# Kernel tuning notes

Hardware: AMD Instinct MI355X
Metric: run time of the kernel (lower is better)

## Reference

```python
import jax, jax.numpy as jnp
import numpy as np

E = 200      # embsize
R = 480      # num relations
T = 8        # cur_ts (history length)
N = 40000    # num entities
B = 1024     # batch of triples
NEG_INF = -1.0e9


def _lin(x, W, b):
    # torch nn.Linear convention: y = x @ W.T + b
    return x @ W.T + b


def _gru_cell(x, h, wih, whh, bih, bhh):
    # torch GRUCell: gates packed as [r, z, n]
    gi = x @ wih.T + bih
    gh = h @ whh.T + bhh
    i_r, i_z, i_n = jnp.split(gi, 3, axis=1)
    h_r, h_z, h_n = jnp.split(gh, 3, axis=1)
    r = jax.nn.sigmoid(i_r + h_r)
    z = jax.nn.sigmoid(i_z + h_z)
    n = jnp.tanh(i_n + r * h_n)
    return (1.0 - z) * n + z * h


def setup_inputs() -> dict:
    key = jax.random.key(0)
    ks = jax.random.split(key, 24)
    s = 0.05
    pre_emb = jax.random.normal(ks[0], (N, E), dtype=jnp.float32)
    r_emb = jax.random.normal(ks[1], (R, E), dtype=jnp.float32)
    partial_embeding = jax.random.randint(ks[2], (B, T * R), 0, 2).astype(jnp.float32)
    sub = jax.random.randint(ks[3], (B,), 0, N)
    rel = jax.random.randint(ks[4], (B,), 0, R)
    obj = jax.random.randint(ks[5], (B,), 0, N)
    all_triples = jnp.stack([sub, rel, obj], axis=1).astype(jnp.int64)
    params = {
        'W1': jax.random.normal(ks[6], (2 * E, E)) * s, 'b1': jnp.zeros((2 * E,)),
        'W2': jax.random.normal(ks[7], (E, 2 * E)) * s, 'b2': jnp.zeros((E,)),
        'Wa': jax.random.normal(ks[8], (E, E)) * s, 'ba': jnp.zeros((E,)),
        'Wh1': jax.random.normal(ks[9], (E, E)) * s, 'bh1': jnp.zeros((E,)),
        'Wh2': jax.random.normal(ks[10], (E, E)) * s, 'bh2': jnp.zeros((E,)),
        'Wal': jax.random.normal(ks[11], (E, E)) * s, 'bal': jnp.zeros((E,)),
        'gru_wih': jax.random.normal(ks[12], (3 * E, E)) * s,
        'gru_whh': jax.random.normal(ks[13], (3 * E, E)) * s,
        'gru_bih': jnp.zeros((3 * E,)),
        'gru_bhh': jnp.zeros((3 * E,)),
    }
    params = {k: v.astype(jnp.float32) for k, v in params.items()}
    out = {'pre_emb': pre_emb, 'r_emb': r_emb, 'partial_embeding': partial_embeding,
           'all_triples': all_triples, 'cur_ts': T, 'num_rel': R}
    out.update(params)
    return out


def reference(pre_emb, r_emb, partial_embeding, all_triples, cur_ts, num_rel,
              W1, b1, W2, b2, Wa, ba, Wh1, bh1, Wh2, bh2, Wal, bal,
              gru_wih, gru_whh, gru_bih, gru_bhh):
    mapped_rel = _lin(_lin(r_emb, W1, b1), W2, b2)          # [R, E]
    q_rel = mapped_rel[all_triples[:, 1]]                    # [B, E]
    b = partial_embeding.shape[0]

    # loop-invariant attention base: linear_attn(q_rel) @ mapped_rel^T -> [B, R]
    base = _lin(q_rel, Wa, ba) @ mapped_rel.T

    # [B, cur_ts*R] -> [cur_ts, B, R] for scan over timesteps
    pe = partial_embeding.reshape(b, cur_ts, num_rel).transpose(1, 0, 2)

    def step(h, cur):
        attn = cur * base
        attn = jnp.where(attn == 0, jnp.float32(NEG_INF), attn)
        a = jax.nn.softmax(attn, axis=1)
        x = a @ mapped_rel                                   # [B, E]
        h = _gru_cell(x, h, gru_wih, gru_whh, gru_bih, gru_bhh)
        return h, None

    h0 = jnp.zeros((b, mapped_rel.shape[1]), dtype=pre_emb.dtype)
    gru_hidden, _ = jax.lax.scan(step, h0, pe)

    predicted_hist = 0.1 * _lin(_lin(q_rel, Wh1, bh1), Wh2, bh2) + q_rel
    match_loss = jnp.mean((predicted_hist - gru_hidden) ** 2)

    # forward_forth (distmult scoring)
    gru_hidden2 = _gru_cell(q_rel, predicted_hist, gru_wih, gru_whh, gru_bih, gru_bhh)
    sub_emb = pre_emb[all_triples[:, 0]]
    score_logits = (_lin(sub_emb, Wal, bal) * gru_hidden2) @ _lin(pre_emb, Wal, bal).T  # [B, N]
    score = jax.nn.sigmoid(score_logits)

    labels = jnp.zeros_like(score_logits).at[jnp.arange(b), all_triples[:, 2]].set(1.0)
    # stable BCE(sigmoid(s), y)
    path_loss = -jnp.mean(labels * jax.nn.log_sigmoid(score_logits)
                          + (1.0 - labels) * jax.nn.log_sigmoid(-score_logits))
    return (match_loss, path_loss, score)
```

## Files before the change

### kernel.cpp

```cpp
#include <hip/hip_runtime.h>
#include <hip/hip_bf16.h>
#include <math.h>

#define EE 200
#define RR 480
#define TT 8
#define NN 40000
#define BB 1024
#define KP 224
#define GP 672
#define GPR 704
#define LDS_STRIDE 232

typedef __attribute__((ext_vector_type(8))) short short8v;
typedef __attribute__((ext_vector_type(4))) float f32x4;

__device__ inline unsigned short f2bf(float x) {
    unsigned int u = __float_as_uint(x);
    unsigned int r = ((u >> 16) & 1u) + 0x7fffu;
    return (unsigned short)((u + r) >> 16);
}
__device__ inline float bf2f(unsigned short h) {
    return __uint_as_float(((unsigned int)h) << 16);
}
__device__ inline float sigm(float x) { return 1.0f / (1.0f + __expf(-x)); }
__device__ inline void split_store(unsigned short* hi, unsigned short* lo, size_t i, float v) {
    unsigned short h = f2bf(v);
    hi[i] = h;
    lo[i] = f2bf(v - bf2f(h));
}

__global__ __launch_bounds__(256) void prep_kernel(
    const float* __restrict__ W1, const float* __restrict__ W2,
    const float* __restrict__ Wa, const float* __restrict__ Wh1,
    const float* __restrict__ Wh2, const float* __restrict__ Wal,
    const float* __restrict__ bal, const float* __restrict__ wih,
    const float* __restrict__ whh, const float* __restrict__ bih,
    const float* __restrict__ bhh,
    unsigned short* W1h, unsigned short* W1l,
    unsigned short* W2h, unsigned short* W2l,
    unsigned short* Wah, unsigned short* Wal_,
    unsigned short* Wh1h, unsigned short* Wh1l,
    unsigned short* Wh2h, unsigned short* Wh2l,
    unsigned short* Walh, unsigned short* Wall,
    unsigned short* WTh, unsigned short* WTl,
    unsigned short* wgh, unsigned short* wgl,
    unsigned short* whg, unsigned short* whl,
    float* bihp, float* bhhp,
    unsigned short* mapSh, unsigned short* mapSl,
    unsigned short* wgiSh, unsigned short* wgiSl,
    unsigned short* hbufs, double* acc)
{
    const int gt = blockIdx.x * 256 + threadIdx.x;
    const int gs = gridDim.x * 256;

    for (int i = gt; i < 448 * 224; i += gs) {
        int r = i / 224, c = i - r * 224;
        split_store(W1h, W1l, i, (r < 400 && c < 200) ? W1[r * 200 + c] : 0.f);
    }
    for (int i = gt; i < 256 * 416; i += gs) {
        int r = i / 416, c = i - r * 416;
        split_store(W2h, W2l, i, (r < 200 && c < 400) ? W2[r * 400 + c] : 0.f);
    }
    for (int i = gt; i < 256 * 224; i += gs) {
        int r = i / 224, c = i - r * 224;
        bool in = (r < 200 && c < 200);
        split_store(Wah,  Wal_, i, in ? Wa[r * 200 + c]  : 0.f);
        split_store(Wh1h, Wh1l, i, in ? Wh1[r * 200 + c] : 0.f);
        split_store(Wh2h, Wh2l, i, in ? Wh2[r * 200 + c] : 0.f);
        split_store(Walh, Wall, i, in ? Wal[r * 200 + c] : 0.f);
        float vt = in ? Wal[c * 200 + r] : ((r == 200 && c < 200) ? bal[c] : 0.f);
        split_store(WTh, WTl, i, vt);
    }
    for (int i = gt; i < 672 * 224; i += gs) {
        int rr = i / 224, c = i - rr * 224;
        int g = rr / 224, j = rr - g * 224;
        bool in = (j < 200 && c < 200);
        split_store(wgh, wgl, i, in ? wih[(size_t)(g * 200 + j) * 200 + c] : 0.f);
        split_store(whg, whl, i, in ? whh[(size_t)(g * 200 + j) * 200 + c] : 0.f);
    }
    for (int i = gt; i < GPR; i += gs) {
        int g = i / 224, j = i - g * 224;
        bihp[i] = (g < 3 && j < 200) ? bih[g * 200 + j] : 0.f;
    }
    for (int i = gt; i < GP; i += gs) {
        int g = i / 224, j = i - g * 224;
        bhhp[i] = (j < 200) ? bhh[g * 200 + j] : 0.f;
    }
    for (int i = gt; i < 512 * 224; i += gs) { mapSh[i] = 0; mapSl[i] = 0; }
    for (int i = gt; i < 704 * 480; i += gs) { wgiSh[i] = 0; wgiSl[i] = 0; }
    for (int i = gt; i < 4 * BB * KP; i += gs) hbufs[i] = 0;
    if (gt == 0) { acc[0] = 0.0; acc[1] = 0.0; }
}

template <int MODE, int OUT, int GATHER, int GATEPAD>
__global__ __launch_bounds__(256) void mfma_flyA(
    const float* __restrict__ A, const int* __restrict__ gidx, int gsel,
    const unsigned short* __restrict__ Bhi, const unsigned short* __restrict__ Blo,
    const float* __restrict__ bias,
    float* __restrict__ Cf, unsigned short* __restrict__ Chi, unsigned short* __restrict__ Clo,
    int M, int N, int Ka, int Ks,
    const float* __restrict__ extra, float alpha, int obf)
{
    const int tid = threadIdx.x;
    const int wave = tid >> 6, lane = tid & 63;
    const int r16 = lane & 15, kq = lane >> 4;
    const int kbase = kq * 8;
    const int bm = blockIdx.y * 64 + wave * 16;
    const int bn = blockIdx.x * 64;

    int arow = bm + r16;
    const bool avalid = arow < M;
    if (GATHER) { if (avalid) arow = gidx[arow * 3 + gsel]; }
    const float* Ap = A + (size_t)arow * Ka;

    f32x4 acc[4] = {{0,0,0,0},{0,0,0,0},{0,0,0,0},{0,0,0,0}};
    const int nk = Ks >> 5;

    for (int kk = 0; kk < nk; kk++) {
        const int k0 = kk * 32 + kbase;
        short8v a0, a1;
        #pragma unroll
        for (int e = 0; e < 8; e++) {
            float v = (avalid && (k0 + e) < Ka) ? Ap[k0 + e] : 0.f;
            unsigned short h = f2bf(v);
            a0[e] = (short)h;
            a1[e] = (short)f2bf(v - bf2f(h));
        }
        #pragma unroll
        for (int nf = 0; nf < 4; nf++) {
            const size_t boff = (size_t)(bn + nf * 16 + r16) * Ks + k0;
            short8v b0 = *(const short8v*)(Bhi + boff);
            short8v b1 = *(const short8v*)(Blo + boff);
            acc[nf] = __builtin_amdgcn_mfma_f32_16x16x32_bf16(a0, b1, acc[nf], 0, 0, 0);
            acc[nf] = __builtin_amdgcn_mfma_f32_16x16x32_bf16(a1, b0, acc[nf], 0, 0, 0);
            acc[nf] = __builtin_amdgcn_mfma_f32_16x16x32_bf16(a0, b0, acc[nf], 0, 0, 0);
        }
    }

    #pragma unroll
    for (int r = 0; r < 4; r++) {
        const int orow = bm + kq * 4 + r;
        if (orow >= M) continue;
        #pragma unroll
        for (int nf = 0; nf < 4; nf++) {
            const int col = bn + nf * 16 + r16;
            float v = acc[nf][r];
            if (OUT == 0) {
                if (col < N) {
                    if (bias) v += bias[col];
                    if (MODE == 1) v = alpha * v + extra[(size_t)orow * N + col];
                    else if (MODE == 2) v = v * extra[(size_t)orow * N + col];
                    Cf[(size_t)orow * N + col] = v;
                }
            } else if (OUT == 1) {
                if (col < obf) {
                    float w = 0.f;
                    if (col < N) { w = v; if (bias) w += bias[col]; }
                    Chi[(size_t)orow * obf + col] = f2bf(w);
                }
            } else if (OUT == 2) {
                if (col < N) {
                    int wr = GATEPAD ? (orow / 200) * 224 + orow % 200 : orow;
                    if (bias) v += bias[col];
                    split_store(Chi, Clo, (size_t)wr * obf + col, v);
                }
            } else if (OUT == 3) {
                if (col < N) {
                    if (bias) v += bias[col];
                    Cf[(size_t)orow * N + col] = v;
                    split_store(Chi, Clo, (size_t)orow * obf + col, v);
                }
            }
        }
    }
}

__global__ __launch_bounds__(256) void mfma_linear3_kernel(
    const unsigned short* __restrict__ Ahi, const unsigned short* __restrict__ Alo,
    const unsigned short* __restrict__ Bhi, const unsigned short* __restrict__ Blo,
    const float* __restrict__ bias, float* __restrict__ C,
    int M, int N, int Ks)
{
    const int tid  = threadIdx.x;
    const int wave = tid >> 6;
    const int lane = tid & 63;
    const int r16   = lane & 15;
    const int khalf = lane >> 4;
    const int kbase = khalf * 8;
    const int bm = blockIdx.y * 64 + wave * 16;
    const int bn = blockIdx.x * 64;

    const unsigned short* ah = Ahi + (size_t)(bm + r16) * Ks + kbase;
    const unsigned short* al = Alo + (size_t)(bm + r16) * Ks + kbase;
    const unsigned short* bh = Bhi + (size_t)(bn + r16) * Ks + kbase;
    const unsigned short* bl = Blo + (size_t)(bn + r16) * Ks + kbase;

    f32x4 acc[4] = {{0,0,0,0},{0,0,0,0},{0,0,0,0},{0,0,0,0}};

    for (int k0 = 0; k0 < Ks; k0 += 32) {
        short8v a0 = *(const short8v*)(ah + k0);
        short8v a1 = *(const short8v*)(al + k0);
        #pragma unroll
        for (int nf = 0; nf < 4; nf++) {
            short8v b0 = *(const short8v*)(bh + (size_t)nf * 16 * Ks + k0);
            short8v b1 = *(const short8v*)(bl + (size_t)nf * 16 * Ks + k0);
            acc[nf] = __builtin_amdgcn_mfma_f32_16x16x32_bf16(a0, b1, acc[nf], 0, 0, 0);
            acc[nf] = __builtin_amdgcn_mfma_f32_16x16x32_bf16(a1, b0, acc[nf], 0, 0, 0);
            acc[nf] = __builtin_amdgcn_mfma_f32_16x16x32_bf16(a0, b0, acc[nf], 0, 0, 0);
        }
    }
    #pragma unroll
    for (int r = 0; r < 4; r++) {
        const int row = bm + khalf * 4 + r;
        #pragma unroll
        for (int nf = 0; nf < 4; nf++) {
            const int col = bn + nf * 16 + r16;
            if (col < N)
                C[(size_t)row * N + col] = acc[nf][r] + (bias ? bias[col] : 0.0f);
        }
    }
}

template <int LAST>
__global__ __launch_bounds__(256) void gru_step_kernel(
    const unsigned short* __restrict__ Whi, const unsigned short* __restrict__ Wlo,
    const float* __restrict__ bhh_pad,
    const float* __restrict__ gi_t,
    const unsigned short* __restrict__ hin_hi, const unsigned short* __restrict__ hin_lo,
    unsigned short* __restrict__ hout_hi, unsigned short* __restrict__ hout_lo,
    float* __restrict__ h_fin)
{
    const int tid = threadIdx.x;
    const int wave = tid >> 6, lane = tid & 63;
    const int r16 = lane & 15, kq = lane >> 4;
    const int jf = blockIdx.x;
    const int brow = (blockIdx.y * 4 + wave) * 16;
    const int j = jf * 16 + r16;

    short8v ahi[7], alo[7];
    const unsigned short* hh = hin_hi + (size_t)(brow + r16) * KP + kq * 8;
    const unsigned short* hl = hin_lo + (size_t)(brow + r16) * KP + kq * 8;
    #pragma unroll
    for (int kk = 0; kk < 7; kk++) {
        ahi[kk] = *(const short8v*)(hh + kk * 32);
        alo[kk] = *(const short8v*)(hl + kk * 32);
    }

    f32x4 ar = {0,0,0,0}, az = {0,0,0,0}, an = {0,0,0,0};
    #pragma unroll
    for (int kk = 0; kk < 7; kk++) {
        const size_t rowr = (size_t)(jf * 16 + r16) * KP + kk * 32 + kq * 8;
        const size_t rowz = rowr + (size_t)224 * KP;
        const size_t rown = rowr + (size_t)448 * KP;
        short8v brh = *(const short8v*)(Whi + rowr);
        short8v brl = *(const short8v*)(Wlo + rowr);
        short8v bzh = *(const short8v*)(Whi + rowz);
        short8v bzl = *(const short8v*)(Wlo + rowz);
        short8v bnh = *(const short8v*)(Whi + rown);
        short8v bnl = *(const short8v*)(Wlo + rown);
        ar = __builtin_amdgcn_mfma_f32_16x16x32_bf16(ahi[kk], brl, ar, 0, 0, 0);
        az = __builtin_amdgcn_mfma_f32_16x16x32_bf16(ahi[kk], bzl, az, 0, 0, 0);
        an = __builtin_amdgcn_mfma_f32_16x16x32_bf16(ahi[kk], bnl, an, 0, 0, 0);
        ar = __builtin_amdgcn_mfma_f32_16x16x32_bf16(alo[kk], brh, ar, 0, 0, 0);
        az = __builtin_amdgcn_mfma_f32_16x16x32_bf16(alo[kk], bzh, az, 0, 0, 0);
        an = __builtin_amdgcn_mfma_f32_16x16x32_bf16(alo[kk], bnh, an, 0, 0, 0);
        ar = __builtin_amdgcn_mfma_f32_16x16x32_bf16(ahi[kk], brh, ar, 0, 0, 0);
        az = __builtin_amdgcn_mfma_f32_16x16x32_bf16(ahi[kk], bzh, az, 0, 0, 0);
        an = __builtin_amdgcn_mfma_f32_16x16x32_bf16(ahi[kk], bnh, an, 0, 0, 0);
    }

    const float br = bhh_pad[j], bz = bhh_pad[224 + j], bn_ = bhh_pad[448 + j];
    #pragma unroll
    for (int q = 0; q < 4; q++) {
        const int row = brow + kq * 4 + q;
        float gir = gi_t[(size_t)row * GP + j];
        float giz = gi_t[(size_t)row * GP + 224 + j];
        float gin = gi_t[(size_t)row * GP + 448 + j];
        float r_ = sigm(gir + ar[q] + br);
        float z_ = sigm(giz + az[q] + bz);
        float n_ = tanhf(gin + r_ * (an[q] + bn_));
        float hold = bf2f(hin_hi[(size_t)row * KP + j]) + bf2f(hin_lo[(size_t)row * KP + j]);
        float hnew = (1.0f - z_) * n_ + z_ * hold;
        if (j < EE) {
            unsigned short nh = f2bf(hnew);
            hout_hi[(size_t)row * KP + j] = nh;
            hout_lo[(size_t)row * KP + j] = f2bf(hnew - bf2f(nh));
            if (LAST) h_fin[(size_t)row * EE + j] = hnew;
        }
    }
}

__global__ __launch_bounds__(256) void gru2_fused_kernel(
    const unsigned short* __restrict__ Wihi, const unsigned short* __restrict__ Wilo,
    const unsigned short* __restrict__ Whhi, const unsigned short* __restrict__ Whlo,
    const float* __restrict__ bih_pad, const float* __restrict__ bhh_pad,
    const float* __restrict__ x, const float* __restrict__ hp,
    float* __restrict__ ghid2)
{
    const int tid = threadIdx.x;
    const int wave = tid >> 6, lane = tid & 63;
    const int r16 = lane & 15, kq = lane >> 4;
    const int jf = blockIdx.x;
    const int brow = (blockIdx.y * 4 + wave) * 16;
    const int j = jf * 16 + r16;

    f32x4 ir = {0,0,0,0}, iz = {0,0,0,0}, in_ = {0,0,0,0};
    f32x4 hr = {0,0,0,0}, hz = {0,0,0,0}, hn = {0,0,0,0};

    {
        const float* xp = x + (size_t)(brow + r16) * EE;
        #pragma unroll
        for (int kk = 0; kk < 7; kk++) {
            short8v a0, a1;
            #pragma unroll
            for (int e = 0; e < 8; e++) {
                int k = kk * 32 + kq * 8 + e;
                float v = (k < EE) ? xp[k] : 0.0f;
                unsigned short hhh = f2bf(v);
                a0[e] = (short)hhh;
                a1[e] = (short)f2bf(v - bf2f(hhh));
            }
            const size_t rowr = (size_t)(jf * 16 + r16) * KP + kk * 32 + kq * 8;
            const size_t rowz = rowr + (size_t)224 * KP;
            const size_t rown = rowr + (size_t)448 * KP;
            short8v brh = *(const short8v*)(Wihi + rowr);
            short8v brl = *(const short8v*)(Wilo + rowr);
            short8v bzh = *(const short8v*)(Wihi + rowz);
            short8v bzl = *(const short8v*)(Wilo + rowz);
            short8v bnh = *(const short8v*)(Wihi + rown);
            short8v bnl = *(const short8v*)(Wilo + rown);
            ir = __builtin_amdgcn_mfma_f32_16x16x32_bf16(a0, brl, ir, 0, 0, 0);
            iz = __builtin_amdgcn_mfma_f32_16x16x32_bf16(a0, bzl, iz, 0, 0, 0);
            in_ = __builtin_amdgcn_mfma_f32_16x16x32_bf16(a0, bnl, in_, 0, 0, 0);
            ir = __builtin_amdgcn_mfma_f32_16x16x32_bf16(a1, brh, ir, 0, 0, 0);
            iz = __builtin_amdgcn_mfma_f32_16x16x32_bf16(a1, bzh, iz, 0, 0, 0);
            in_ = __builtin_amdgcn_mfma_f32_16x16x32_bf16(a1, bnh, in_, 0, 0, 0);
            ir = __builtin_amdgcn_mfma_f32_16x16x32_bf16(a0, brh, ir, 0, 0, 0);
            iz = __builtin_amdgcn_mfma_f32_16x16x32_bf16(a0, bzh, iz, 0, 0, 0);
            in_ = __builtin_amdgcn_mfma_f32_16x16x32_bf16(a0, bnh, in_, 0, 0, 0);
        }
    }
    {
        const float* hpp = hp + (size_t)(brow + r16) * EE;
        #pragma unroll
        for (int kk = 0; kk < 7; kk++) {
            short8v a0, a1;
            #pragma unroll
            for (int e = 0; e < 8; e++) {
                int k = kk * 32 + kq * 8 + e;
                float v = (k < EE) ? hpp[k] : 0.0f;
                unsigned short hhh = f2bf(v);
                a0[e] = (short)hhh;
                a1[e] = (short)f2bf(v - bf2f(hhh));
            }
            const size_t rowr = (size_t)(jf * 16 + r16) * KP + kk * 32 + kq * 8;
            const size_t rowz = rowr + (size_t)224 * KP;
            const size_t rown = rowr + (size_t)448 * KP;
            short8v brh = *(const short8v*)(Whhi + rowr);
            short8v brl = *(const short8v*)(Whlo + rowr);
            short8v bzh = *(const short8v*)(Whhi + rowz);
            short8v bzl = *(const short8v*)(Whlo + rowz);
            short8v bnh = *(const short8v*)(Whhi + rown);
            short8v bnl = *(const short8v*)(Whlo + rown);
            hr = __builtin_amdgcn_mfma_f32_16x16x32_bf16(a0, brl, hr, 0, 0, 0);
            hz = __builtin_amdgcn_mfma_f32_16x16x32_bf16(a0, bzl, hz, 0, 0, 0);
            hn = __builtin_amdgcn_mfma_f32_16x16x32_bf16(a0, bnl, hn, 0, 0, 0);
            hr = __builtin_amdgcn_mfma_f32_16x16x32_bf16(a1, brh, hr, 0, 0, 0);
            hz = __builtin_amdgcn_mfma_f32_16x16x32_bf16(a1, bzh, hz, 0, 0, 0);
            hn = __builtin_amdgcn_mfma_f32_16x16x32_bf16(a1, bnh, hn, 0, 0, 0);
            hr = __builtin_amdgcn_mfma_f32_16x16x32_bf16(a0, brh, hr, 0, 0, 0);
            hz = __builtin_amdgcn_mfma_f32_16x16x32_bf16(a0, bzh, hz, 0, 0, 0);
            hn = __builtin_amdgcn_mfma_f32_16x16x32_bf16(a0, bnh, hn, 0, 0, 0);
        }
    }

    if (j >= EE) return;
    const float bir = bih_pad[j], biz = bih_pad[224 + j], bin = bih_pad[448 + j];
    const float bhr = bhh_pad[j], bhz = bhh_pad[224 + j], bhn = bhh_pad[448 + j];
    #pragma unroll
    for (int q = 0; q < 4; q++) {
        const int row = brow + kq * 4 + q;
        float r_ = sigm(ir[q] + bir + hr[q] + bhr);
        float z_ = sigm(iz[q] + biz + hz[q] + bhz);
        float n_ = tanhf(in_[q] + bin + r_ * (hn[q] + bhn));
        float hold = hp[(size_t)row * EE + j];
        ghid2[(size_t)row * EE + j] = (1.0f - z_) * n_ + z_ * hold;
    }
}

__global__ __launch_bounds__(256) void score_mfma2_kernel(
    const unsigned short* __restrict__ Ubf,
    const float* __restrict__ pre_emb,
    const int* __restrict__ triples,
    float* __restrict__ outScore,
    double* __restrict__ accPath)
{
    __shared__ unsigned short Bs[64 * LDS_STRIDE];
    __shared__ int objs[BB];
    __shared__ float red[256];

    const int tid = threadIdx.x;
    const int bn = blockIdx.x * 64;

    for (int i = tid; i < BB; i += 256) objs[i] = triples[i * 3 + 2];

    for (int idx = tid; idx < 64 * 50; idx += 256) {
        int row = idx / 50;
        int c4 = (idx - row * 50) * 4;
        float4 v = *(const float4*)(pre_emb + (size_t)(bn + row) * EE + c4);
        unsigned short* d = &Bs[row * LDS_STRIDE + c4];
        d[0] = f2bf(v.x); d[1] = f2bf(v.y); d[2] = f2bf(v.z); d[3] = f2bf(v.w);
    }
    for (int idx = tid; idx < 64 * 24; idx += 256) {
        int row = idx / 24;
        int cc = idx - row * 24;
        Bs[row * LDS_STRIDE + 200 + cc] = (cc == 0) ? (unsigned short)0x3F80 : (unsigned short)0;
    }
    __syncthreads();

    const int wave  = tid >> 6;
    const int lane  = tid & 63;
    const int r16   = lane & 15;
    const int khalf = lane >> 4;
    const int kbase = khalf * 8;

    const unsigned short* bs0 = &Bs[( 0 + r16) * LDS_STRIDE + kbase];
    const unsigned short* bs1 = &Bs[(16 + r16) * LDS_STRIDE + kbase];
    const unsigned short* bs2 = &Bs[(32 + r16) * LDS_STRIDE + kbase];
    const unsigned short* bs3 = &Bs[(48 + r16) * LDS_STRIDE + kbase];

    float psum = 0.0f;

    for (int m0 = 0; m0 < BB; m0 += 64) {
        const unsigned short* Ap = Ubf + (size_t)(m0 + wave * 16 + r16) * KP + kbase;
        f32x4 acc0 = {0,0,0,0}, acc1 = {0,0,0,0}, acc2 = {0,0,0,0}, acc3 = {0,0,0,0};
        #pragma unroll
        for (int k0 = 0; k0 < KP; k0 += 32) {
            short8v a  = *(const short8v*)(Ap + k0);
            short8v b0 = *(const short8v*)(bs0 + k0);
            short8v b1 = *(const short8v*)(bs1 + k0);
            short8v b2 = *(const short8v*)(bs2 + k0);
            short8v b3 = *(const short8v*)(bs3 + k0);
            acc0 = __builtin_amdgcn_mfma_f32_16x16x32_bf16(a, b0, acc0, 0, 0, 0);
            acc1 = __builtin_amdgcn_mfma_f32_16x16x32_bf16(a, b1, acc1, 0, 0, 0);
            acc2 = __builtin_amdgcn_mfma_f32_16x16x32_bf16(a, b2, acc2, 0, 0, 0);
            acc3 = __builtin_amdgcn_mfma_f32_16x16x32_bf16(a, b3, acc3, 0, 0, 0);
        }
        #pragma unroll
        for (int r = 0; r < 4; r++) {
            const int grow = m0 + wave * 16 + khalf * 4 + r;
            const int objc = objs[grow];
            float xv[4] = { acc0[r], acc1[r], acc2[r], acc3[r] };
            #pragma unroll
            for (int nf = 0; nf < 4; nf++) {
                const int col = bn + nf * 16 + r16;
                float x  = xv[nf];
                float e  = __expf(-fabsf(x));
                float t1 = 1.0f + e;
                float rc = __builtin_amdgcn_rcpf(t1);
                float sig = (x >= 0.0f) ? rc : e * rc;
                float sp = __logf(t1);
                float s  = (col == objc) ? x : -x;
                psum += fminf(s, 0.0f) - sp;
                outScore[(size_t)grow * NN + col] = sig;
            }
        }
    }
    red[tid] = psum;
    __syncthreads();
    for (int s = 128; s > 0; s >>= 1) {
        if (tid < s) red[tid] += red[tid + s];
        __syncthreads();
    }
    if (tid == 0) atomicAdd(accPath, (double)red[0]);
}

__global__ __launch_bounds__(256) void masked_softmax_all_kernel(
    const float* __restrict__ base, const float* __restrict__ part,
    unsigned short* __restrict__ aout_hi, unsigned short* __restrict__ aout_lo)
{
    __shared__ float sv[RR];
    __shared__ float red[256];
    const int blk = blockIdx.x;
    const int b = blk & (BB - 1);
    const int t = blk >> 10;
    const int tid = threadIdx.x;
    const float* brow = base + (size_t)b * RR;
    const float* prow = part + (size_t)b * (TT * RR) + t * RR;

    float lmax = -3.0e38f;
    for (int r = tid; r < RR; r += 256) {
        float v = prow[r] * brow[r];
        if (v == 0.0f) v = -1000000000.0f;
        sv[r] = v;
        lmax = fmaxf(lmax, v);
    }
    red[tid] = lmax;
    __syncthreads();
    for (int s = 128; s > 0; s >>= 1) {
        if (tid < s) red[tid] = fmaxf(red[tid], red[tid + s]);
        __syncthreads();
    }
    float gmax = red[0];
    __syncthreads();

    float lsum = 0.0f;
    for (int r = tid; r < RR; r += 256) {
        float e = __expf(sv[r] - gmax);
        sv[r] = e;
        lsum += e;
    }
    red[tid] = lsum;
    __syncthreads();
    for (int s = 128; s > 0; s >>= 1) {
        if (tid < s) red[tid] += red[tid + s];
        __syncthreads();
    }
    float inv = 1.0f / red[0];
    for (int r = tid; r < RR; r += 256) {
        float w = sv[r] * inv;
        unsigned short h = f2bf(w);
        aout_hi[(size_t)blk * RR + r] = h;
        aout_lo[(size_t)blk * RR + r] = f2bf(w - bf2f(h));
    }
}

__global__ __launch_bounds__(256) void gather_rows_kernel(
    const float* __restrict__ src, const int* __restrict__ idx,
    int idxStride, int idxOff, float* __restrict__ dst, int rows, int cols)
{
    int i = blockIdx.x * 256 + threadIdx.x;
    if (i >= rows * cols) return;
    int r = i / cols, c = i - r * cols;
    dst[i] = src[(size_t)idx[r * idxStride + idxOff] * cols + c];
}

__global__ __launch_bounds__(256) void sqdiff_reduce_kernel(
    const float* __restrict__ a, const float* __restrict__ b, int n,
    double* __restrict__ acc)
{
    __shared__ float red[256];
    int tid = threadIdx.x;
    float s = 0.0f;
    for (int i = blockIdx.x * 256 + tid; i < n; i += gridDim.x * 256) {
        float d = a[i] - b[i];
        s += d * d;
    }
    red[tid] = s;
    __syncthreads();
    for (int st = 128; st > 0; st >>= 1) {
        if (tid < st) red[tid] += red[tid + st];
        __syncthreads();
    }
    if (tid == 0) atomicAdd(acc, (double)red[0]);
}

__global__ void final_kernel(const double* __restrict__ acc, float* __restrict__ out)
{
    if (threadIdx.x == 0) {
        out[0] = (float)(acc[0] / ((double)BB * EE));
        out[1] = (float)(-acc[1] / ((double)BB * NN));
    }
}

extern "C" void kernel_launch(void* const* d_in, const int* in_sizes, int n_in,
                              void* d_out, int out_size, void* d_ws, size_t ws_size,
                              hipStream_t stream) {
    const float* pre_emb = (const float*)d_in[0];
    const float* r_emb   = (const float*)d_in[1];
    const float* part    = (const float*)d_in[2];
    const int*   triples = (const int*)d_in[3];
    const float* W1  = (const float*)d_in[6];
    const float* b1  = (const float*)d_in[7];
    const float* W2  = (const float*)d_in[8];
    const float* b2  = (const float*)d_in[9];
    const float* Wa  = (const float*)d_in[10];
    const float* ba  = (const float*)d_in[11];
    const float* Wh1 = (const float*)d_in[12];
    const float* bh1 = (const float*)d_in[13];
    const float* Wh2 = (const float*)d_in[14];
    const float* bh2 = (const float*)d_in[15];
    const float* Wal = (const float*)d_in[16];
    const float* bal = (const float*)d_in[17];
    const float* wih = (const float*)d_in[18];
    const float* whh = (const float*)d_in[19];
    const float* bih = (const float*)d_in[20];
    const float* bhh = (const float*)d_in[21];

    float* out = (float*)d_out;
    double* acc = (double*)d_ws;
    float* wsf = (float*)d_ws;
    size_t off = 4;
    auto alloc = [&](size_t n) { float* p = wsf + off; off += (n + 3) & ~(size_t)3; return p; };
    auto allocS = [&](size_t n) { return (unsigned short*)alloc((n + 1) / 2); };

    unsigned short* W1h  = allocS((size_t)448 * 224);
    unsigned short* W1l  = allocS((size_t)448 * 224);
    unsigned short* W2h  = allocS((size_t)256 * 416);
    unsigned short* W2l  = allocS((size_t)256 * 416);
    unsigned short* Wah  = allocS((size_t)256 * 224);
    unsigned short* Wal_ = allocS((size_t)256 * 224);
    unsigned short* Wh1h = allocS((size_t)256 * 224);
    unsigned short* Wh1l = allocS((size_t)256 * 224);
    unsigned short* Wh2h = allocS((size_t)256 * 224);
    unsigned short* Wh2l = allocS((size_t)256 * 224);
    unsigned short* Walh = allocS((size_t)256 * 224);
    unsigned short* Wall = allocS((size_t)256 * 224);
    unsigned short* WTh  = allocS((size_t)256 * 224);
    unsigned short* WTl  = allocS((size_t)256 * 224);
    unsigned short* wihg_h = allocS((size_t)GP * KP);
    unsigned short* wihg_l = allocS((size_t)GP * KP);
    unsigned short* whhg_h = allocS((size_t)GP * KP);
    unsigned short* whhg_l = allocS((size_t)GP * KP);
    float* bihp = alloc(GPR);
    float* bhhp = alloc(GP);
    unsigned short* mapSh = allocS((size_t)512 * 224);
    unsigned short* mapSl = allocS((size_t)512 * 224);
    unsigned short* wgiSh = allocS((size_t)GPR * RR);
    unsigned short* wgiSl = allocS((size_t)GPR * RR);
    unsigned short* hbufs = allocS((size_t)4 * BB * KP);
    unsigned short* ha_hi = hbufs;
    unsigned short* ha_lo = hbufs + (size_t)BB * KP;
    unsigned short* hb_hi = hbufs + (size_t)2 * BB * KP;
    unsigned short* hb_lo = hbufs + (size_t)3 * BB * KP;

    float* h1     = alloc((size_t)RR * 400);
    float* map    = alloc((size_t)RR * EE);
    float* qrel   = alloc((size_t)BB * EE);
    float* qa     = alloc((size_t)BB * EE);
    float* basep  = alloc((size_t)BB * RR);
    unsigned short* aw_hi = allocS((size_t)TT * BB * RR);
    unsigned short* aw_lo = allocS((size_t)TT * BB * RR);
    float* gi_all = alloc((size_t)TT * BB * GP);
    float* hfin   = alloc((size_t)BB * EE);
    float* ph1    = alloc((size_t)BB * EE);
    float* pred   = alloc((size_t)BB * EE);
    float* ghid2  = alloc((size_t)BB * EE);
    float* s1h    = alloc((size_t)BB * EE);
    unsigned short* u_bf = allocS((size_t)BB * KP);

    dim3 blk(256);

    prep_kernel<<<1024, blk, 0, stream>>>(
        W1, W2, Wa, Wh1, Wh2, Wal, bal, wih, whh, bih, bhh,
        W1h, W1l, W2h, W2l, Wah, Wal_, Wh1h, Wh1l, Wh2h, Wh2l, Walh, Wall,
        WTh, WTl, wihg_h, wihg_l, whhg_h, whhg_l, bihp, bhhp,
        mapSh, mapSl, wgiSh, wgiSl, hbufs, acc);

    mfma_flyA<0,0,0,0><<<dim3(7, 8), blk, 0, stream>>>(
        r_emb, nullptr, 0, W1h, W1l, b1, h1, nullptr, nullptr,
        RR, 400, EE, 224, nullptr, 0.f, 0);
    mfma_flyA<0,3,0,0><<<dim3(4, 8), blk, 0, stream>>>(
        h1, nullptr, 0, W2h, W2l, b2, map, mapSh, mapSl,
        RR, EE, 400, 416, nullptr, 0.f, 224);
    gather_rows_kernel<<<((BB * EE) + 255) / 256, blk, 0, stream>>>(map, triples, 3, 1, qrel, BB, EE);
    mfma_flyA<0,0,1,0><<<dim3(4, 16), blk, 0, stream>>>(
        map, triples, 1, Wah, Wal_, ba, qa, nullptr, nullptr,
        BB, EE, EE, 224, nullptr, 0.f, 0);
    mfma_flyA<0,0,0,0><<<dim3(8, 16), blk, 0, stream>>>(
        qa, nullptr, 0, mapSh, mapSl, nullptr, basep, nullptr, nullptr,
        BB, RR, EE, 224, nullptr, 0.f, 0);
    masked_softmax_all_kernel<<<TT * BB, blk, 0, stream>>>(basep, part, aw_hi, aw_lo);
    mfma_flyA<0,2,0,1><<<dim3(8, 10), blk, 0, stream>>>(
        wih, nullptr, 0, mapSh, mapSl, nullptr, nullptr, wgiSh, wgiSl,
        600, RR, EE, 224, nullptr, 0.f, RR);
    mfma_linear3_kernel<<<dim3(11, TT * BB / 64), blk, 0, stream>>>(
        aw_hi, aw_lo, wgiSh, wgiSl, bihp, gi_all, TT * BB, GP, RR);

    for (int t = 0; t < TT; t++) {
        const float* gi_t = gi_all + (size_t)t * BB * GP;
        const unsigned short* ih = (t & 1) ? hb_hi : ha_hi;
        const unsigned short* il = (t & 1) ? hb_lo : ha_lo;
        unsigned short* oh = (t & 1) ? ha_hi : hb_hi;
        unsigned short* ol = (t & 1) ? ha_lo : hb_lo;
        if (t == TT - 1)
            gru_step_kernel<1><<<dim3(13, BB / 64), blk, 0, stream>>>(
                whhg_h, whhg_l, bhhp, gi_t, ih, il, oh, ol, hfin);
        else
            gru_step_kernel<0><<<dim3(13, BB / 64), blk, 0, stream>>>(
                whhg_h, whhg_l, bhhp, gi_t, ih, il, oh, ol, nullptr);
    }

    mfma_flyA<0,0,1,0><<<dim3(4, 16), blk, 0, stream>>>(
        map, triples, 1, Wh1h, Wh1l, bh1, ph1, nullptr, nullptr,
        BB, EE, EE, 224, nullptr, 0.f, 0);
    mfma_flyA<1,0,0,0><<<dim3(4, 16), blk, 0, stream>>>(
        ph1, nullptr, 0, Wh2h, Wh2l, bh2, pred, nullptr, nullptr,
        BB, EE, EE, 224, qrel, 0.1f, 0);
    sqdiff_reduce_kernel<<<128, blk, 0, stream>>>(pred, hfin, BB * EE, acc + 0);
    gru2_fused_kernel<<<dim3(13, BB / 64), blk, 0, stream>>>(
        wihg_h, wihg_l, whhg_h, whhg_l, bihp, bhhp, qrel, pred, ghid2);
    mfma_flyA<2,0,1,0><<<dim3(4, 16), blk, 0, stream>>>(
        pre_emb, triples, 0, Walh, Wall, bal, s1h, nullptr, nullptr,
        BB, EE, EE, 224, ghid2, 0.f, 0);
    mfma_flyA<0,1,0,0><<<dim3(4, 16), blk, 0, stream>>>(
        s1h, nullptr, 0, WTh, WTl, nullptr, nullptr, u_bf, nullptr,
        BB, KP, EE, 224, nullptr, 0.f, KP);
    score_mfma2_kernel<<<NN / 64, blk, 0, stream>>>(u_bf, pre_emb, triples, out + 2, acc + 1);
    final_kernel<<<1, 64, 0, stream>>>(acc, out);
}
```

Measured before the change: 467.0 us.

## Fuse small launches, drop softmax low-part precision, widen score kernel blocks

Merges the Wa and Wh1 projections into one GEMM with a concatenated weight, folds the qrel gather into the consumers (gathered extra and gru2 input), and fuses the match-loss squared-difference reduction into the gru2 kernel. It also drops the bf16 low part of the attention weights, turning a 3-MFMA split into 2, and doubles the score kernel block to 512 threads. The intent is fewer launches and less memory traffic. In exchange the softmax-weighted GRU input loses some precision.

```diff
diff --git a/kernel.cpp b/kernel.cpp
--- a/kernel.cpp
+++ b/kernel.cpp
@@ -30,77 +30,83 @@
     lo[i] = f2bf(v - bf2f(h));
 }
 
+struct PrepPtrs {
+    unsigned short *W1h, *W1l, *W2h, *W2l, *Wabh, *Wabl, *Wh2h, *Wh2l;
+    unsigned short *Walh, *Wall, *WTh, *WTl, *wgh, *wgl, *whg, *whl;
+    float *bab, *bihp, *bhhp;
+    unsigned short *mapSh, *mapSl, *wgiSh, *wgiSl, *hbufs;
+    double* acc;
+};
+
 __global__ __launch_bounds__(256) void prep_kernel(
     const float* __restrict__ W1, const float* __restrict__ W2,
     const float* __restrict__ Wa, const float* __restrict__ Wh1,
     const float* __restrict__ Wh2, const float* __restrict__ Wal,
     const float* __restrict__ bal, const float* __restrict__ wih,
-    const float* __restrict__ whh, const float* __restrict__ bih,
-    const float* __restrict__ bhh,
-    unsigned short* W1h, unsigned short* W1l,
-    unsigned short* W2h, unsigned short* W2l,
-    unsigned short* Wah, unsigned short* Wal_,
-    unsigned short* Wh1h, unsigned short* Wh1l,
-    unsigned short* Wh2h, unsigned short* Wh2l,
-    unsigned short* Walh, unsigned short* Wall,
-    unsigned short* WTh, unsigned short* WTl,
-    unsigned short* wgh, unsigned short* wgl,
-    unsigned short* whg, unsigned short* whl,
-    float* bihp, float* bhhp,
-    unsigned short* mapSh, unsigned short* mapSl,
-    unsigned short* wgiSh, unsigned short* wgiSl,
-    unsigned short* hbufs, double* acc)
+    const float* __restrict__ whh, const float* __restrict__ ba,
+    const float* __restrict__ bh1, const float* __restrict__ bih,
+    const float* __restrict__ bhh, PrepPtrs p)
 {
     const int gt = blockIdx.x * 256 + threadIdx.x;
     const int gs = gridDim.x * 256;
 
     for (int i = gt; i < 448 * 224; i += gs) {
         int r = i / 224, c = i - r * 224;
-        split_store(W1h, W1l, i, (r < 400 && c < 200) ? W1[r * 200 + c] : 0.f);
+        split_store(p.W1h, p.W1l, i, (r < 400 && c < 200) ? W1[r * 200 + c] : 0.f);
+        float vab = 0.f;
+        if (c < 200) {
+            if (r < 200) vab = Wa[r * 200 + c];
+            else if (r >= 224 && r < 424) vab = Wh1[(r - 224) * 200 + c];
+        }
+        split_store(p.Wabh, p.Wabl, i, vab);
     }
     for (int i = gt; i < 256 * 416; i += gs) {
         int r = i / 416, c = i - r * 416;
-        split_store(W2h, W2l, i, (r < 200 && c < 400) ? W2[r * 400 + c] : 0.f);
+        split_store(p.W2h, p.W2l, i, (r < 200 && c < 400) ? W2[r * 400 + c] : 0.f);
     }
     for (int i = gt; i < 256 * 224; i += gs) {
         int r = i / 224, c = i - r * 224;
         bool in = (r < 200 && c < 200);
-        split_store(Wah,  Wal_, i, in ? Wa[r * 200 + c]  : 0.f);
-        split_store(Wh1h, Wh1l, i, in ? Wh1[r * 200 + c] : 0.f);
-        split_store(Wh2h, Wh2l, i, in ? Wh2[r * 200 + c] : 0.f);
-        split_store(Walh, Wall, i, in ? Wal[r * 200 + c] : 0.f);
+        split_store(p.Wh2h, p.Wh2l, i, in ? Wh2[r * 200 + c] : 0.f);
+        split_store(p.Walh, p.Wall, i, in ? Wal[r * 200 + c] : 0.f);
         float vt = in ? Wal[c * 200 + r] : ((r == 200 && c < 200) ? bal[c] : 0.f);
-        split_store(WTh, WTl, i, vt);
+        split_store(p.WTh, p.WTl, i, vt);
     }
     for (int i = gt; i < 672 * 224; i += gs) {
         int rr = i / 224, c = i - rr * 224;
         int g = rr / 224, j = rr - g * 224;
         bool in = (j < 200 && c < 200);
-        split_store(wgh, wgl, i, in ? wih[(size_t)(g * 200 + j) * 200 + c] : 0.f);
-        split_store(whg, whl, i, in ? whh[(size_t)(g * 200 + j) * 200 + c] : 0.f);
+        split_store(p.wgh, p.wgl, i, in ? wih[(size_t)(g * 200 + j) * 200 + c] : 0.f);
+        split_store(p.whg, p.whl, i, in ? whh[(size_t)(g * 200 + j) * 200 + c] : 0.f);
+    }
+    for (int i = gt; i < 448; i += gs) {
+        float v = 0.f;
+        if (i < 200) v = ba[i];
+        else if (i >= 224 && i < 424) v = bh1[i - 224];
+        p.bab[i] = v;
     }
     for (int i = gt; i < GPR; i += gs) {
         int g = i / 224, j = i - g * 224;
-        bihp[i] = (g < 3 && j < 200) ? bih[g * 200 + j] : 0.f;
+        p.bihp[i] = (g < 3 && j < 200) ? bih[g * 200 + j] : 0.f;
     }
     for (int i = gt; i < GP; i += gs) {
         int g = i / 224, j = i - g * 224;
-        bhhp[i] = (j < 200) ? bhh[g * 200 + j] : 0.f;
-    }
-    for (int i = gt; i < 512 * 224; i += gs) { mapSh[i] = 0; mapSl[i] = 0; }
-    for (int i = gt; i < 704 * 480; i += gs) { wgiSh[i] = 0; wgiSl[i] = 0; }
-    for (int i = gt; i < 4 * BB * KP; i += gs) hbufs[i] = 0;
-    if (gt == 0) { acc[0] = 0.0; acc[1] = 0.0; }
-}
-
-template <int MODE, int OUT, int GATHER, int GATEPAD>
+        p.bhhp[i] = (j < 200) ? bhh[g * 200 + j] : 0.f;
+    }
+    for (int i = gt; i < 512 * 224; i += gs) { p.mapSh[i] = 0; p.mapSl[i] = 0; }
+    for (int i = gt; i < 704 * 480; i += gs) { p.wgiSh[i] = 0; p.wgiSl[i] = 0; }
+    for (int i = gt; i < 4 * BB * KP; i += gs) p.hbufs[i] = 0;
+    if (gt == 0) { p.acc[0] = 0.0; p.acc[1] = 0.0; }
+}
+
+template <int MODE, int OUT, int GATHER, int GATEPAD, int EGATHER>
 __global__ __launch_bounds__(256) void mfma_flyA(
-    const float* __restrict__ A, const int* __restrict__ gidx, int gsel,
+    const float* __restrict__ A, int lda, const int* __restrict__ gidx, int gsel,
     const unsigned short* __restrict__ Bhi, const unsigned short* __restrict__ Blo,
     const float* __restrict__ bias,
     float* __restrict__ Cf, unsigned short* __restrict__ Chi, unsigned short* __restrict__ Clo,
     int M, int N, int Ka, int Ks,
-    const float* __restrict__ extra, float alpha, int obf)
+    const float* __restrict__ extra, int eld, float alpha, int obf)
 {
     const int tid = threadIdx.x;
     const int wave = tid >> 6, lane = tid & 63;
@@ -112,7 +118,7 @@
     int arow = bm + r16;
     const bool avalid = arow < M;
     if (GATHER) { if (avalid) arow = gidx[arow * 3 + gsel]; }
-    const float* Ap = A + (size_t)arow * Ka;
+    const float* Ap = A + (size_t)arow * lda;
 
     f32x4 acc[4] = {{0,0,0,0},{0,0,0,0},{0,0,0,0},{0,0,0,0}};
     const int nk = Ks >> 5;
@@ -149,8 +155,13 @@
             if (OUT == 0) {
                 if (col < N) {
                     if (bias) v += bias[col];
-                    if (MODE == 1) v = alpha * v + extra[(size_t)orow * N + col];
-                    else if (MODE == 2) v = v * extra[(size_t)orow * N + col];
+                    if (MODE == 1) {
+                        float ex = EGATHER ? extra[(size_t)gidx[orow * 3 + gsel] * eld + col]
+                                           : extra[(size_t)orow * eld + col];
+                        v = alpha * v + ex;
+                    } else if (MODE == 2) {
+                        v = v * extra[(size_t)orow * eld + col];
+                    }
                     Cf[(size_t)orow * N + col] = v;
                 }
             } else if (OUT == 1) {
@@ -176,8 +187,8 @@
     }
 }
 
-__global__ __launch_bounds__(256) void mfma_linear3_kernel(
-    const unsigned short* __restrict__ Ahi, const unsigned short* __restrict__ Alo,
+__global__ __launch_bounds__(256) void mfma_linear2_kernel(
+    const unsigned short* __restrict__ Ahi,
     const unsigned short* __restrict__ Bhi, const unsigned short* __restrict__ Blo,
     const float* __restrict__ bias, float* __restrict__ C,
     int M, int N, int Ks)
@@ -192,7 +203,6 @@
     const int bn = blockIdx.x * 64;
 
     const unsigned short* ah = Ahi + (size_t)(bm + r16) * Ks + kbase;
-    const unsigned short* al = Alo + (size_t)(bm + r16) * Ks + kbase;
     const unsigned short* bh = Bhi + (size_t)(bn + r16) * Ks + kbase;
     const unsigned short* bl = Blo + (size_t)(bn + r16) * Ks + kbase;
 
@@ -200,13 +210,11 @@
 
     for (int k0 = 0; k0 < Ks; k0 += 32) {
         short8v a0 = *(const short8v*)(ah + k0);
-        short8v a1 = *(const short8v*)(al + k0);
         #pragma unroll
         for (int nf = 0; nf < 4; nf++) {
             short8v b0 = *(const short8v*)(bh + (size_t)nf * 16 * Ks + k0);
             short8v b1 = *(const short8v*)(bl + (size_t)nf * 16 * Ks + k0);
             acc[nf] = __builtin_amdgcn_mfma_f32_16x16x32_bf16(a0, b1, acc[nf], 0, 0, 0);
-            acc[nf] = __builtin_amdgcn_mfma_f32_16x16x32_bf16(a1, b0, acc[nf], 0, 0, 0);
             acc[nf] = __builtin_amdgcn_mfma_f32_16x16x32_bf16(a0, b0, acc[nf], 0, 0, 0);
         }
     }
@@ -295,9 +303,11 @@
     const unsigned short* __restrict__ Wihi, const unsigned short* __restrict__ Wilo,
     const unsigned short* __restrict__ Whhi, const unsigned short* __restrict__ Whlo,
     const float* __restrict__ bih_pad, const float* __restrict__ bhh_pad,
-    const float* __restrict__ x, const float* __restrict__ hp,
-    float* __restrict__ ghid2)
-{
+    const int* __restrict__ triples, const float* __restrict__ map,
+    const float* __restrict__ hp, const float* __restrict__ hfin,
+    float* __restrict__ ghid2, double* __restrict__ accMatch)
+{
+    __shared__ float red[256];
     const int tid = threadIdx.x;
     const int wave = tid >> 6, lane = tid & 63;
     const int r16 = lane & 15, kq = lane >> 4;
@@ -309,7 +319,8 @@
     f32x4 hr = {0,0,0,0}, hz = {0,0,0,0}, hn = {0,0,0,0};
 
     {
-        const float* xp = x + (size_t)(brow + r16) * EE;
+        const int xrow = triples[(brow + r16) * 3 + 1];
+        const float* xp = map + (size_t)xrow * EE;
         #pragma unroll
         for (int kk = 0; kk < 7; kk++) {
             short8v a0, a1;
@@ -375,21 +386,32 @@
         }
     }
 
-    if (j >= EE) return;
-    const float bir = bih_pad[j], biz = bih_pad[224 + j], bin = bih_pad[448 + j];
-    const float bhr = bhh_pad[j], bhz = bhh_pad[224 + j], bhn = bhh_pad[448 + j];
-    #pragma unroll
-    for (int q = 0; q < 4; q++) {
-        const int row = brow + kq * 4 + q;
-        float r_ = sigm(ir[q] + bir + hr[q] + bhr);
-        float z_ = sigm(iz[q] + biz + hz[q] + bhz);
-        float n_ = tanhf(in_[q] + bin + r_ * (hn[q] + bhn));
-        float hold = hp[(size_t)row * EE + j];
-        ghid2[(size_t)row * EE + j] = (1.0f - z_) * n_ + z_ * hold;
-    }
-}
-
-__global__ __launch_bounds__(256) void score_mfma2_kernel(
+    float psum = 0.0f;
+    if (j < EE) {
+        const float bir = bih_pad[j], biz = bih_pad[224 + j], bin = bih_pad[448 + j];
+        const float bhr = bhh_pad[j], bhz = bhh_pad[224 + j], bhn = bhh_pad[448 + j];
+        #pragma unroll
+        for (int q = 0; q < 4; q++) {
+            const int row = brow + kq * 4 + q;
+            float r_ = sigm(ir[q] + bir + hr[q] + bhr);
+            float z_ = sigm(iz[q] + biz + hz[q] + bhz);
+            float n_ = tanhf(in_[q] + bin + r_ * (hn[q] + bhn));
+            float hold = hp[(size_t)row * EE + j];
+            ghid2[(size_t)row * EE + j] = (1.0f - z_) * n_ + z_ * hold;
+            float d = hold - hfin[(size_t)row * EE + j];
+            psum += d * d;
+        }
+    }
+    red[tid] = psum;
+    __syncthreads();
+    for (int s = 128; s > 0; s >>= 1) {
+        if (tid < s) red[tid] += red[tid + s];
+        __syncthreads();
+    }
+    if (tid == 0) atomicAdd(accMatch, (double)red[0]);
+}
+
+__global__ __launch_bounds__(512) void score_mfma2_kernel(
     const unsigned short* __restrict__ Ubf,
     const float* __restrict__ pre_emb,
     const int* __restrict__ triples,
@@ -398,21 +420,21 @@
 {
     __shared__ unsigned short Bs[64 * LDS_STRIDE];
     __shared__ int objs[BB];
-    __shared__ float red[256];
+    __shared__ float red[512];
 
     const int tid = threadIdx.x;
     const int bn = blockIdx.x * 64;
 
-    for (int i = tid; i < BB; i += 256) objs[i] = triples[i * 3 + 2];
-
-    for (int idx = tid; idx < 64 * 50; idx += 256) {
+    for (int i = tid; i < BB; i += 512) objs[i] = triples[i * 3 + 2];
+
+    for (int idx = tid; idx < 64 * 50; idx += 512) {
         int row = idx / 50;
         int c4 = (idx - row * 50) * 4;
         float4 v = *(const float4*)(pre_emb + (size_t)(bn + row) * EE + c4);
         unsigned short* d = &Bs[row * LDS_STRIDE + c4];
         d[0] = f2bf(v.x); d[1] = f2bf(v.y); d[2] = f2bf(v.z); d[3] = f2bf(v.w);
     }
-    for (int idx = tid; idx < 64 * 24; idx += 256) {
+    for (int idx = tid; idx < 64 * 24; idx += 512) {
         int row = idx / 24;
         int cc = idx - row * 24;
         Bs[row * LDS_STRIDE + 200 + cc] = (cc == 0) ? (unsigned short)0x3F80 : (unsigned short)0;
@@ -432,8 +454,9 @@
 
     float psum = 0.0f;
 
-    for (int m0 = 0; m0 < BB; m0 += 64) {
-        const unsigned short* Ap = Ubf + (size_t)(m0 + wave * 16 + r16) * KP + kbase;
+    for (int mi = 0; mi < 8; mi++) {
+        const int m0 = mi * 128 + wave * 16;
+        const unsigned short* Ap = Ubf + (size_t)(m0 + r16) * KP + kbase;
         f32x4 acc0 = {0,0,0,0}, acc1 = {0,0,0,0}, acc2 = {0,0,0,0}, acc3 = {0,0,0,0};
         #pragma unroll
         for (int k0 = 0; k0 < KP; k0 += 32) {
@@ -449,7 +472,7 @@
         }
         #pragma unroll
         for (int r = 0; r < 4; r++) {
-            const int grow = m0 + wave * 16 + khalf * 4 + r;
+            const int grow = m0 + khalf * 4 + r;
             const int objc = objs[grow];
             float xv[4] = { acc0[r], acc1[r], acc2[r], acc3[r] };
             #pragma unroll
@@ -469,7 +492,7 @@
     }
     red[tid] = psum;
     __syncthreads();
-    for (int s = 128; s > 0; s >>= 1) {
+    for (int s = 256; s > 0; s >>= 1) {
         if (tid < s) red[tid] += red[tid + s];
         __syncthreads();
     }
@@ -478,7 +501,7 @@
 
 __global__ __launch_bounds__(256) void masked_softmax_all_kernel(
     const float* __restrict__ base, const float* __restrict__ part,
-    unsigned short* __restrict__ aout_hi, unsigned short* __restrict__ aout_lo)
+    unsigned short* __restrict__ aout_hi)
 {
     __shared__ float sv[RR];
     __shared__ float red[256];
@@ -518,42 +541,8 @@
         __syncthreads();
     }
     float inv = 1.0f / red[0];
-    for (int r = tid; r < RR; r += 256) {
-        float w = sv[r] * inv;
-        unsigned short h = f2bf(w);
-        aout_hi[(size_t)blk * RR + r] = h;
-        aout_lo[(size_t)blk * RR + r] = f2bf(w - bf2f(h));
-    }
-}
-
-__global__ __launch_bounds__(256) void gather_rows_kernel(
-    const float* __restrict__ src, const int* __restrict__ idx,
-    int idxStride, int idxOff, float* __restrict__ dst, int rows, int cols)
-{
-    int i = blockIdx.x * 256 + threadIdx.x;
-    if (i >= rows * cols) return;
-    int r = i / cols, c = i - r * cols;
-    dst[i] = src[(size_t)idx[r * idxStride + idxOff] * cols + c];
-}
-
-__global__ __launch_bounds__(256) void sqdiff_reduce_kernel(
-    const float* __restrict__ a, const float* __restrict__ b, int n,
-    double* __restrict__ acc)
-{
-    __shared__ float red[256];
-    int tid = threadIdx.x;
-    float s = 0.0f;
-    for (int i = blockIdx.x * 256 + tid; i < n; i += gridDim.x * 256) {
-        float d = a[i] - b[i];
-        s += d * d;
-    }
-    red[tid] = s;
-    __syncthreads();
-    for (int st = 128; st > 0; st >>= 1) {
-        if (tid < st) red[tid] += red[tid + st];
-        __syncthreads();
-    }
-    if (tid == 0) atomicAdd(acc, (double)red[0]);
+    for (int r = tid; r < RR; r += 256)
+        aout_hi[(size_t)blk * RR + r] = f2bf(sv[r] * inv);
 }
 
 __global__ void final_kernel(const double* __restrict__ acc, float* __restrict__ out)
@@ -595,46 +584,45 @@
     auto alloc = [&](size_t n) { float* p = wsf + off; off += (n + 3) & ~(size_t)3; return p; };
     auto allocS = [&](size_t n) { return (unsigned short*)alloc((n + 1) / 2); };
 
-    unsigned short* W1h  = allocS((size_t)448 * 224);
-    unsigned short* W1l  = allocS((size_t)448 * 224);
-    unsigned short* W2h  = allocS((size_t)256 * 416);
-    unsigned short* W2l  = allocS((size_t)256 * 416);
-    unsigned short* Wah  = allocS((size_t)256 * 224);
-    unsigned short* Wal_ = allocS((size_t)256 * 224);
-    unsigned short* Wh1h = allocS((size_t)256 * 224);
-    unsigned short* Wh1l = allocS((size_t)256 * 224);
-    unsigned short* Wh2h = allocS((size_t)256 * 224);
-    unsigned short* Wh2l = allocS((size_t)256 * 224);
-    unsigned short* Walh = allocS((size_t)256 * 224);
-    unsigned short* Wall = allocS((size_t)256 * 224);
-    unsigned short* WTh  = allocS((size_t)256 * 224);
-    unsigned short* WTl  = allocS((size_t)256 * 224);
-    unsigned short* wihg_h = allocS((size_t)GP * KP);
-    unsigned short* wihg_l = allocS((size_t)GP * KP);
-    unsigned short* whhg_h = allocS((size_t)GP * KP);
-    unsigned short* whhg_l = allocS((size_t)GP * KP);
-    float* bihp = alloc(GPR);
-    float* bhhp = alloc(GP);
-    unsigned short* mapSh = allocS((size_t)512 * 224);
-    unsigned short* mapSl = allocS((size_t)512 * 224);
-    unsigned short* wgiSh = allocS((size_t)GPR * RR);
-    unsigned short* wgiSl = allocS((size_t)GPR * RR);
-    unsigned short* hbufs = allocS((size_t)4 * BB * KP);
-    unsigned short* ha_hi = hbufs;
-    unsigned short* ha_lo = hbufs + (size_t)BB * KP;
-    unsigned short* hb_hi = hbufs + (size_t)2 * BB * KP;
-    unsigned short* hb_lo = hbufs + (size_t)3 * BB * KP;
+    PrepPtrs p;
+    p.W1h  = allocS((size_t)448 * 224);
+    p.W1l  = allocS((size_t)448 * 224);
+    p.W2h  = allocS((size_t)256 * 416);
+    p.W2l  = allocS((size_t)256 * 416);
+    p.Wabh = allocS((size_t)448 * 224);
+    p.Wabl = allocS((size_t)448 * 224);
+    p.Wh2h = allocS((size_t)256 * 224);
+    p.Wh2l = allocS((size_t)256 * 224);
+    p.Walh = allocS((size_t)256 * 224);
+    p.Wall = allocS((size_t)256 * 224);
+    p.WTh  = allocS((size_t)256 * 224);
+    p.WTl  = allocS((size_t)256 * 224);
+    p.wgh  = allocS((size_t)GP * KP);
+    p.wgl  = allocS((size_t)GP * KP);
+    p.whg  = allocS((size_t)GP * KP);
+    p.whl  = allocS((size_t)GP * KP);
+    p.bab  = alloc(448);
+    p.bihp = alloc(GPR);
+    p.bhhp = alloc(GP);
+    p.mapSh = allocS((size_t)512 * 224);
+    p.mapSl = allocS((size_t)512 * 224);
+    p.wgiSh = allocS((size_t)GPR * RR);
+    p.wgiSl = allocS((size_t)GPR * RR);
+    p.hbufs = allocS((size_t)4 * BB * KP);
+    p.acc = acc;
+
+    unsigned short* ha_hi = p.hbufs;
+    unsigned short* ha_lo = p.hbufs + (size_t)BB * KP;
+    unsigned short* hb_hi = p.hbufs + (size_t)2 * BB * KP;
+    unsigned short* hb_lo = p.hbufs + (size_t)3 * BB * KP;
 
     float* h1     = alloc((size_t)RR * 400);
     float* map    = alloc((size_t)RR * EE);
-    float* qrel   = alloc((size_t)BB * EE);
-    float* qa     = alloc((size_t)BB * EE);
+    float* qa_ph1 = alloc((size_t)BB * 448);
     float* basep  = alloc((size_t)BB * RR);
     unsigned short* aw_hi = allocS((size_t)TT * BB * RR);
-    unsigned short* aw_lo = allocS((size_t)TT * BB * RR);
     float* gi_all = alloc((size_t)TT * BB * GP);
     float* hfin   = alloc((size_t)BB * EE);
-    float* ph1    = alloc((size_t)BB * EE);
     float* pred   = alloc((size_t)BB * EE);
     float* ghid2  = alloc((size_t)BB * EE);
     float* s1h    = alloc((size_t)BB * EE);
@@ -643,30 +631,26 @@
     dim3 blk(256);
 
     prep_kernel<<<1024, blk, 0, stream>>>(
-        W1, W2, Wa, Wh1, Wh2, Wal, bal, wih, whh, bih, bhh,
-        W1h, W1l, W2h, W2l, Wah, Wal_, Wh1h, Wh1l, Wh2h, Wh2l, Walh, Wall,
-        WTh, WTl, wihg_h, wihg_l, whhg_h, whhg_l, bihp, bhhp,
-        mapSh, mapSl, wgiSh, wgiSl, hbufs, acc);
-
-    mfma_flyA<0,0,0,0><<<dim3(7, 8), blk, 0, stream>>>(
-        r_emb, nullptr, 0, W1h, W1l, b1, h1, nullptr, nullptr,
-        RR, 400, EE, 224, nullptr, 0.f, 0);
-    mfma_flyA<0,3,0,0><<<dim3(4, 8), blk, 0, stream>>>(
-        h1, nullptr, 0, W2h, W2l, b2, map, mapSh, mapSl,
-        RR, EE, 400, 416, nullptr, 0.f, 224);
-    gather_rows_kernel<<<((BB * EE) + 255) / 256, blk, 0, stream>>>(map, triples, 3, 1, qrel, BB, EE);
-    mfma_flyA<0,0,1,0><<<dim3(4, 16), blk, 0, stream>>>(
-        map, triples, 1, Wah, Wal_, ba, qa, nullptr, nullptr,
-        BB, EE, EE, 224, nullptr, 0.f, 0);
-    mfma_flyA<0,0,0,0><<<dim3(8, 16), blk, 0, stream>>>(
-        qa, nullptr, 0, mapSh, mapSl, nullptr, basep, nullptr, nullptr,
-        BB, RR, EE, 224, nullptr, 0.f, 0);
-    masked_softmax_all_kernel<<<TT * BB, blk, 0, stream>>>(basep, part, aw_hi, aw_lo);
-    mfma_flyA<0,2,0,1><<<dim3(8, 10), blk, 0, stream>>>(
-        wih, nullptr, 0, mapSh, mapSl, nullptr, nullptr, wgiSh, wgiSl,
-        600, RR, EE, 224, nullptr, 0.f, RR);
-    mfma_linear3_kernel<<<dim3(11, TT * BB / 64), blk, 0, stream>>>(
-        aw_hi, aw_lo, wgiSh, wgiSl, bihp, gi_all, TT * BB, GP, RR);
+        W1, W2, Wa, Wh1, Wh2, Wal, bal, wih, whh, ba, bh1, bih, bhh, p);
+
+    mfma_flyA<0,0,0,0,0><<<dim3(7, 8), blk, 0, stream>>>(
+        r_emb, 200, nullptr, 0, p.W1h, p.W1l, b1, h1, nullptr, nullptr,
+        RR, 400, 200, 224, nullptr, 0, 0.f, 0);
+    mfma_flyA<0,3,0,0,0><<<dim3(4, 8), blk, 0, stream>>>(
+        h1, 400, nullptr, 0, p.W2h, p.W2l, b2, map, p.mapSh, p.mapSl,
+        RR, EE, 400, 416, nullptr, 0, 0.f, 224);
+    mfma_flyA<0,0,1,0,0><<<dim3(7, 16), blk, 0, stream>>>(
+        map, 200, triples, 1, p.Wabh, p.Wabl, p.bab, qa_ph1, nullptr, nullptr,
+        BB, 448, 200, 224, nullptr, 0, 0.f, 0);
+    mfma_flyA<0,0,0,0,0><<<dim3(8, 16), blk, 0, stream>>>(
+        qa_ph1, 448, nullptr, 0, p.mapSh, p.mapSl, nullptr, basep, nullptr, nullptr,
+        BB, RR, 200, 224, nullptr, 0, 0.f, 0);
+    masked_softmax_all_kernel<<<TT * BB, blk, 0, stream>>>(basep, part, aw_hi);
+    mfma_flyA<0,2,0,1,0><<<dim3(8, 10), blk, 0, stream>>>(
+        wih, 200, nullptr, 0, p.mapSh, p.mapSl, nullptr, nullptr, p.wgiSh, p.wgiSl,
+        600, RR, 200, 224, nullptr, 0, 0.f, RR);
+    mfma_linear2_kernel<<<dim3(11, TT * BB / 64), blk, 0, stream>>>(
+        aw_hi, p.wgiSh, p.wgiSl, p.bihp, gi_all, TT * BB, GP, RR);
 
     for (int t = 0; t < TT; t++) {
         const float* gi_t = gi_all + (size_t)t * BB * GP;
@@ -676,27 +660,24 @@
         unsigned short* ol = (t & 1) ? ha_lo : hb_lo;
         if (t == TT - 1)
             gru_step_kernel<1><<<dim3(13, BB / 64), blk, 0, stream>>>(
-                whhg_h, whhg_l, bhhp, gi_t, ih, il, oh, ol, hfin);
+                p.whg, p.whl, p.bhhp, gi_t, ih, il, oh, ol, hfin);
         else
             gru_step_kernel<0><<<dim3(13, BB / 64), blk, 0, stream>>>(
-                whhg_h, whhg_l, bhhp, gi_t, ih, il, oh, ol, nullptr);
-    }
-
-    mfma_flyA<0,0,1,0><<<dim3(4, 16), blk, 0, stream>>>(
-        map, triples, 1, Wh1h, Wh1l, bh1, ph1, nullptr, nullptr,
-        BB, EE, EE, 224, nullptr, 0.f, 0);
-    mfma_flyA<1,0,0,0><<<dim3(4, 16), blk, 0, stream>>>(
-        ph1, nullptr, 0, Wh2h, Wh2l, bh2, pred, nullptr, nullptr,
-        BB, EE, EE, 224, qrel, 0.1f, 0);
-    sqdiff_reduce_kernel<<<128, blk, 0, stream>>>(pred, hfin, BB * EE, acc + 0);
+                p.whg, p.whl, p.bhhp, gi_t, ih, il, oh, ol, nullptr);
+    }
+
+    mfma_flyA<1,0,0,0,1><<<dim3(4, 16), blk, 0, stream>>>(
+        qa_ph1 + 224, 448, triples, 1, p.Wh2h, p.Wh2l, bh2, pred, nullptr, nullptr,
+        BB, EE, 200, 224, map, 200, 0.1f, 0);
     gru2_fused_kernel<<<dim3(13, BB / 64), blk, 0, stream>>>(
-        wihg_h, wihg_l, whhg_h, whhg_l, bihp, bhhp, qrel, pred, ghid2);
-    mfma_flyA<2,0,1,0><<<dim3(4, 16), blk, 0, stream>>>(
-        pre_emb, triples, 0, Walh, Wall, bal, s1h, nullptr, nullptr,
-        BB, EE, EE, 224, ghid2, 0.f, 0);
-    mfma_flyA<0,1,0,0><<<dim3(4, 16), blk, 0, stream>>>(
-        s1h, nullptr, 0, WTh, WTl, nullptr, nullptr, u_bf, nullptr,
-        BB, KP, EE, 224, nullptr, 0.f, KP);
-    score_mfma2_kernel<<<NN / 64, blk, 0, stream>>>(u_bf, pre_emb, triples, out + 2, acc + 1);
+        p.wgh, p.wgl, p.whg, p.whl, p.bihp, p.bhhp,
+        triples, map, pred, hfin, ghid2, acc + 0);
+    mfma_flyA<2,0,1,0,0><<<dim3(4, 16), blk, 0, stream>>>(
+        pre_emb, 200, triples, 0, p.Walh, p.Wall, bal, s1h, nullptr, nullptr,
+        BB, EE, 200, 224, ghid2, 200, 0.f, 0);
+    mfma_flyA<0,1,0,0,0><<<dim3(4, 16), blk, 0, stream>>>(
+        s1h, 200, nullptr, 0, p.WTh, p.WTl, nullptr, nullptr, u_bf, nullptr,
+        BB, KP, 200, 224, nullptr, 0, 0.f, KP);
+    score_mfma2_kernel<<<NN / 64, dim3(512), 0, stream>>>(u_bf, pre_emb, triples, out + 2, acc + 1);
     final_kernel<<<1, 64, 0, stream>>>(acc, out);
 }
```

New measurement: 442.1 us. 5.3% less time.
